# Kernel tuning notes

Hardware: AMD Instinct MI355X
Metric: run time of the kernel (lower is better)

The kernel has to match this reference:

```python
import jax, jax.numpy as jnp
import numpy as np

B, N, C = 4, 4096, 256
GROUPS = 50
M_SCALE = 10.0


def setup_inputs() -> dict:
    key = jax.random.key(0)
    ks = jax.random.split(key, 6)
    s = 0.02
    return {
        "inputs": jax.random.normal(ks[0], (B, N, 1, C), dtype=jnp.float32),
        "W_sem": jax.random.normal(ks[1], (C, 128), dtype=jnp.float32) * s,
        "b_sem": jnp.zeros((128,), jnp.float32),
        "W_seg": jax.random.normal(ks[2], (128, GROUPS), dtype=jnp.float32) * s,
        "b_seg": jnp.zeros((GROUPS,), jnp.float32),
        "W_sim": jax.random.normal(ks[3], (C, 128), dtype=jnp.float32) * s,
        "b_sim": jnp.zeros((128,), jnp.float32),
        "W_conf": jax.random.normal(ks[4], (C, 128), dtype=jnp.float32) * s,
        "b_conf": jnp.zeros((128,), jnp.float32),
        "W_cl": jax.random.normal(ks[5], (128, 1), dtype=jnp.float32) * s,
        "b_cl": jnp.zeros((1,), jnp.float32),
    }


def reference(inputs, W_sem, b_sem, W_seg, b_seg, W_sim, b_sim,
              W_conf, b_conf, W_cl, b_cl):
    # 1x1 Conv2D on [B, N, 1, C] == per-point dense layer on channels.
    x = inputs[:, :, 0, :]  # [B, N, C]

    # Semantic segmentation head
    Fsem = jnp.einsum('bnc,cd->bnd', x, W_sem) + b_sem          # [B, N, 128]
    ptssemseg_logits = jnp.einsum('bnd,dg->bng', Fsem, W_seg) + b_seg  # [B, N, G]
    ptssemseg = jax.nn.softmax(ptssemseg_logits, axis=-1)

    # Similarity head: pairwise squared distances of Fsim rows
    Fsim = jnp.einsum('bnc,cd->bnd', x, W_sim) + b_sim          # [B, N, 128]
    r = jnp.sum(Fsim * Fsim, axis=2)                             # [B, N]
    gram = jnp.einsum('bnd,bmd->bnm', Fsim, Fsim)                # [B, N, N]
    D = r[:, :, None] - 2.0 * gram + r[:, None, :]               # [B, N, N]
    simmat_logits = jnp.maximum(M_SCALE * D, 0.0)

    # Confidence head
    Fconf = jnp.einsum('bnc,cd->bnd', x, W_conf) + b_conf        # [B, N, 128]
    conf_logits = jnp.einsum('bnd,do->bno', Fconf, W_cl) + b_cl  # [B, N, 1]
    conf = jax.nn.sigmoid(conf_logits)

    return (ptssemseg, ptssemseg_logits, simmat_logits, conf, conf_logits)
```

## Files before the change

kernel.cpp:

```cpp
#include <hip/hip_runtime.h>
#include <cstdint>
#include <cstddef>

#define NN 4096
#define CC 256
#define GG 50

#define O_OUT1 819200
#define O_OUT2 1638400
#define O_OUT3 68747264
#define O_OUT4 68763648

typedef _Float16 half8 __attribute__((ext_vector_type(8)));
typedef float f32x4 __attribute__((ext_vector_type(4)));
typedef short short8 __attribute__((ext_vector_type(8)));

__device__ __forceinline__ unsigned bf16b(float f) {
    unsigned u = __float_as_uint(f);
    return (u + 0x7FFFu + ((u >> 16) & 1u)) >> 16;
}
__device__ __forceinline__ float bf16f(short s) {
    return __uint_as_float(((unsigned)(unsigned short)s) << 16);
}

__global__ __launch_bounds__(256) void k_proj(
    const float* __restrict__ x,
    const float* __restrict__ Wsem, const float* __restrict__ bsem,
    const float* __restrict__ Wseg, const float* __restrict__ bseg,
    const float* __restrict__ Wsim, const float* __restrict__ bsim,
    const float* __restrict__ Wconf, const float* __restrict__ bconf,
    const float* __restrict__ Wcl, const float* __restrict__ bcl,
    unsigned* __restrict__ fsimu, float* __restrict__ rnorm,
    float* __restrict__ out0, float* __restrict__ out1,
    float* __restrict__ out3, float* __restrict__ out4)
{
    __shared__ float hsem[64 * 132];
    __shared__ float confl[64], rns[64];

    int t = threadIdx.x;
    int lane = t & 63, wv = t >> 6;
    int rowl = lane & 15, quad = lane >> 4;
    int pbase = blockIdx.x * 64;

    if (t < 64) { confl[t] = 0.f; rns[t] = 0.f; }

    const float* wcol[6];
    #pragma unroll
    for (int jf = 0; jf < 6; ++jf) {
        int j384 = (wv * 6 + jf) * 16 + rowl;
        const float* m = (j384 < 128) ? Wsim : (j384 < 256) ? Wsem : Wconf;
        wcol[jf] = m + (j384 & 127);
    }
    const float* xrow[4];
    #pragma unroll
    for (int pf = 0; pf < 4; ++pf)
        xrow[pf] = x + (size_t)(pbase + pf * 16 + rowl) * CC;

    f32x4 acc[6][4];
    #pragma unroll
    for (int jf = 0; jf < 6; ++jf)
        #pragma unroll
        for (int pf = 0; pf < 4; ++pf) { f32x4 z = {0.f,0.f,0.f,0.f}; acc[jf][pf] = z; }

    #pragma unroll 2
    for (int kc = 0; kc < 8; ++kc) {
        half8 A[6];
        #pragma unroll
        for (int jf = 0; jf < 6; ++jf) {
            const float* wp = wcol[jf] + (size_t)(kc * 32 + quad * 8) * 128;
            #pragma unroll
            for (int e = 0; e < 8; ++e) A[jf][e] = (_Float16)wp[(size_t)e * 128];
        }
        half8 Bv[4];
        #pragma unroll
        for (int pf = 0; pf < 4; ++pf) {
            const float* xp = xrow[pf] + kc * 32 + quad * 8;
            float4 x0 = *(const float4*)xp;
            float4 x1 = *(const float4*)(xp + 4);
            Bv[pf][0] = (_Float16)x0.x; Bv[pf][1] = (_Float16)x0.y;
            Bv[pf][2] = (_Float16)x0.z; Bv[pf][3] = (_Float16)x0.w;
            Bv[pf][4] = (_Float16)x1.x; Bv[pf][5] = (_Float16)x1.y;
            Bv[pf][6] = (_Float16)x1.z; Bv[pf][7] = (_Float16)x1.w;
        }
        #pragma unroll
        for (int pf = 0; pf < 4; ++pf)
            #pragma unroll
            for (int jf = 0; jf < 6; ++jf)
                acc[jf][pf] = __builtin_amdgcn_mfma_f32_16x16x32_f16(A[jf], Bv[pf], acc[jf][pf], 0, 0, 0);
    }

    __syncthreads();

    float rsum[4] = {0.f,0.f,0.f,0.f};
    float csum[4] = {0.f,0.f,0.f,0.f};
    bool hasSim = (wv * 6 < 8);
    bool hasConf = (wv * 6 + 5 >= 16);

    #pragma unroll
    for (int jf = 0; jf < 6; ++jf) {
        int jfg = wv * 6 + jf;
        int j0 = jfg * 16 + quad * 4;
        const float* barr = (j0 < 128) ? (bsim + j0)
                          : (j0 < 256) ? (bsem + (j0 - 128)) : (bconf + (j0 - 256));
        float4 b4 = *(const float4*)barr;
        if (jfg < 8) {
            #pragma unroll
            for (int pf = 0; pf < 4; ++pf) {
                int pt = pf * 16 + rowl;
                f32x4 v = acc[jf][pf];
                unsigned p0 = bf16b(v[0] + b4.x) | (bf16b(v[1] + b4.y) << 16);
                unsigned p1 = bf16b(v[2] + b4.z) | (bf16b(v[3] + b4.w) << 16);
                *(uint2*)&fsimu[(size_t)(pbase + pt) * 64 + jfg * 8 + quad * 2] = make_uint2(p0, p1);
                float f0 = bf16f((short)(p0 & 0xFFFF)), f1 = bf16f((short)(p0 >> 16));
                float f2 = bf16f((short)(p1 & 0xFFFF)), f3 = bf16f((short)(p1 >> 16));
                rsum[pf] += f0*f0 + f1*f1 + f2*f2 + f3*f3;
            }
        } else if (jfg < 16) {
            #pragma unroll
            for (int pf = 0; pf < 4; ++pf) {
                int pt = pf * 16 + rowl;
                f32x4 v = acc[jf][pf];
                f32x4 o;
                o[0] = v[0] + b4.x; o[1] = v[1] + b4.y; o[2] = v[2] + b4.z; o[3] = v[3] + b4.w;
                *(f32x4*)&hsem[pt * 132 + (jfg - 8) * 16 + quad * 4] = o;
            }
        } else {
            float4 w4 = *(const float4*)&Wcl[(jfg - 16) * 16 + quad * 4];
            #pragma unroll
            for (int pf = 0; pf < 4; ++pf) {
                f32x4 v = acc[jf][pf];
                csum[pf] += (v[0] + b4.x) * w4.x + (v[1] + b4.y) * w4.y
                          + (v[2] + b4.z) * w4.z + (v[3] + b4.w) * w4.w;
            }
        }
    }
    if (hasSim) {
        #pragma unroll
        for (int pf = 0; pf < 4; ++pf) atomicAdd(&rns[pf * 16 + rowl], rsum[pf]);
    }
    if (hasConf) {
        #pragma unroll
        for (int pf = 0; pf < 4; ++pf) atomicAdd(&confl[pf * 16 + rowl], csum[pf]);
    }
    __syncthreads();

    if (t < 64) {
        float cl = confl[t] + bcl[0];
        out4[pbase + t] = cl;
        out3[pbase + t] = 1.f / (1.f + __expf(-cl));
        rnorm[pbase + t] = rns[t];
    }

    half8 As[4][4];
    #pragma unroll
    for (int gf = 0; gf < 4; ++gf) {
        int gg = gf * 16 + rowl;
        #pragma unroll
        for (int k2 = 0; k2 < 4; ++k2)
            #pragma unroll
            for (int e = 0; e < 8; ++e) {
                int d = k2 * 32 + quad * 8 + e;
                As[gf][k2][e] = (gg < GG) ? (_Float16)Wseg[(size_t)d * GG + gg] : (_Float16)0.f;
            }
    }
    f32x4 sacc[4];
    #pragma unroll
    for (int gf = 0; gf < 4; ++gf) { f32x4 z = {0.f,0.f,0.f,0.f}; sacc[gf] = z; }
    #pragma unroll
    for (int k2 = 0; k2 < 4; ++k2) {
        const float* hp = &hsem[(wv * 16 + rowl) * 132 + k2 * 32 + quad * 8];
        half8 Bh;
        #pragma unroll
        for (int e = 0; e < 8; ++e) Bh[e] = (_Float16)hp[e];
        #pragma unroll
        for (int gf = 0; gf < 4; ++gf)
            sacc[gf] = __builtin_amdgcn_mfma_f32_16x16x32_f16(As[gf][k2], Bh, sacc[gf], 0, 0, 0);
    }

    float l[4][4];
    float mx = -1e30f;
    #pragma unroll
    for (int gf = 0; gf < 4; ++gf)
        #pragma unroll
        for (int e = 0; e < 4; ++e) {
            int g = gf * 16 + quad * 4 + e;
            float lv = (g < GG) ? sacc[gf][e] + bseg[g] : -1e30f;
            l[gf][e] = lv;
            mx = fmaxf(mx, lv);
        }
    mx = fmaxf(mx, __shfl_xor(mx, 16));
    mx = fmaxf(mx, __shfl_xor(mx, 32));
    float s = 0.f;
    #pragma unroll
    for (int gf = 0; gf < 4; ++gf)
        #pragma unroll
        for (int e = 0; e < 4; ++e) {
            int g = gf * 16 + quad * 4 + e;
            if (g < GG) s += __expf(l[gf][e] - mx);
        }
    s += __shfl_xor(s, 16);
    s += __shfl_xor(s, 32);
    float inv = 1.f / s;

    size_t orow = (size_t)(pbase + wv * 16 + rowl) * GG;
    #pragma unroll
    for (int gf = 0; gf < 4; ++gf)
        #pragma unroll
        for (int e = 0; e < 4; ++e) {
            int g = gf * 16 + quad * 4 + e;
            if (g < GG) {
                out1[orow + g] = l[gf][e];
                out0[orow + g] = __expf(l[gf][e] - mx) * inv;
            }
        }
}

__global__ __launch_bounds__(256) void k_simmat(
    const short* __restrict__ fs, const float* __restrict__ rn, float* __restrict__ out2)
{
    int t = threadIdx.x;
    int lane = t & 63, wv = t >> 6;
    int b = blockIdx.y;

    int p = blockIdx.x;
    int tj = (int)((sqrtf((float)(8 * p + 1)) - 1.f) * 0.5f);
    while ((tj + 1) * (tj + 2) / 2 <= p) ++tj;
    while (tj * (tj + 1) / 2 > p) --tj;
    int ti = p - tj * (tj + 1) / 2;

    int I = ti * 128 + (wv >> 1) * 64;
    int J = tj * 128 + (wv & 1) * 64;
    int rowl = lane & 15, quad = lane >> 4;

    const short8* F = (const short8*)(fs + (size_t)b * NN * 128);
    const float* rb = rn + b * NN;

    f32x4 acc[4][4];
    #pragma unroll
    for (int r = 0; r < 4; ++r)
        #pragma unroll
        for (int c = 0; c < 4; ++c) { f32x4 z = {0.f,0.f,0.f,0.f}; acc[r][c] = z; }

    #pragma unroll
    for (int s = 0; s < 4; ++s) {
        short8 av[4], bv[4];
        #pragma unroll
        for (int r = 0; r < 4; ++r)
            av[r] = F[(size_t)(I + r * 16 + rowl) * 16 + s * 4 + quad];
        #pragma unroll
        for (int c = 0; c < 4; ++c)
            bv[c] = F[(size_t)(J + c * 16 + rowl) * 16 + s * 4 + quad];
        #pragma unroll
        for (int r = 0; r < 4; ++r)
            #pragma unroll
            for (int c = 0; c < 4; ++c)
                acc[r][c] = __builtin_amdgcn_mfma_f32_16x16x32_bf16(av[r], bv[c], acc[r][c], 0, 0, 0);
    }

    f32x4 rI4[4];
    float rJs[4];
    #pragma unroll
    for (int r = 0; r < 4; ++r)
        rI4[r] = *(const f32x4*)&rb[I + r * 16 + quad * 4];
    #pragma unroll
    for (int c = 0; c < 4; ++c)
        rJs[c] = rb[J + c * 16 + rowl];

    #pragma unroll
    for (int r = 0; r < 4; ++r)
        #pragma unroll
        for (int c = 0; c < 4; ++c) {
            f32x4 v = acc[r][c];
            float rj = rJs[c];
            f32x4 o;
            #pragma unroll
            for (int e = 0; e < 4; ++e)
                o[e] = fmaxf(10.f * (rI4[r][e] + rj) - 20.f * v[e], 0.f);
            acc[r][c] = o;
        }

    float* ob = out2 + (size_t)b * NN * NN;

    #pragma unroll
    for (int r = 0; r < 4; ++r) {
        int rbase = I + r * 16 + quad * 4;
        #pragma unroll
        for (int c = 0; c < 4; ++c) {
            int col = J + c * 16 + rowl;
            f32x4 v = acc[r][c];
            #pragma unroll
            for (int e = 0; e < 4; ++e)
                __builtin_nontemporal_store(v[e], &ob[(size_t)(rbase + e) * NN + col]);
        }
    }

    if (ti != tj) {
        #pragma unroll
        for (int c = 0; c < 4; ++c) {
            size_t rowoff = (size_t)(J + c * 16 + rowl) * NN;
            #pragma unroll
            for (int r = 0; r < 4; ++r)
                __builtin_nontemporal_store(acc[r][c],
                    (f32x4*)&ob[rowoff + (I + r * 16 + quad * 4)]);
        }
    }
}

extern "C" void kernel_launch(void* const* d_in, const int* in_sizes, int n_in,
                              void* d_out, int out_size, void* d_ws, size_t ws_size,
                              hipStream_t stream)
{
    const float* x     = (const float*)d_in[0];
    const float* Wsem  = (const float*)d_in[1];
    const float* bsem  = (const float*)d_in[2];
    const float* Wseg  = (const float*)d_in[3];
    const float* bseg  = (const float*)d_in[4];
    const float* Wsim  = (const float*)d_in[5];
    const float* bsim  = (const float*)d_in[6];
    const float* Wconf = (const float*)d_in[7];
    const float* bconf = (const float*)d_in[8];
    const float* Wcl   = (const float*)d_in[9];
    const float* bcl   = (const float*)d_in[10];

    const size_t FSIM_BYTES = (size_t)4 * NN * 128 * 2;
    if (ws_size < FSIM_BYTES + (size_t)4 * NN * sizeof(float)) return;
    unsigned* fsim = (unsigned*)d_ws;
    float* rnorm = (float*)((char*)d_ws + FSIM_BYTES);

    float* out  = (float*)d_out;
    float* out0 = out;
    float* out1 = out + O_OUT1;
    float* out2 = out + O_OUT2;
    float* out3 = out + O_OUT3;
    float* out4 = out + O_OUT4;

    hipLaunchKernelGGL(k_proj, dim3(256), dim3(256), 0, stream,
                       x, Wsem, bsem, Wseg, bseg, Wsim, bsim, Wconf, bconf, Wcl, bcl,
                       fsim, rnorm, out0, out1, out3, out4);
    hipLaunchKernelGGL(k_simmat, dim3(528, 4, 1), dim3(256), 0, stream,
                       (const short*)fsim, rnorm, out2);
}
```

Before: 357.9 us.

## Compute full row strips of simmat and stage through LDS for coalesced stores

Measured after the change: 415.5 us. 16.1% more time.

```diff
diff --git a/kernel.cpp b/kernel.cpp
--- a/kernel.cpp
+++ b/kernel.cpp
@@ -218,91 +218,67 @@
 __global__ __launch_bounds__(256) void k_simmat(
     const short* __restrict__ fs, const float* __restrict__ rn, float* __restrict__ out2)
 {
+    __shared__ float tile[16 * 516];
+
     int t = threadIdx.x;
     int lane = t & 63, wv = t >> 6;
+    int rowl = lane & 15, quad = lane >> 4;
     int b = blockIdx.y;
-
-    int p = blockIdx.x;
-    int tj = (int)((sqrtf((float)(8 * p + 1)) - 1.f) * 0.5f);
-    while ((tj + 1) * (tj + 2) / 2 <= p) ++tj;
-    while (tj * (tj + 1) / 2 > p) --tj;
-    int ti = p - tj * (tj + 1) / 2;
-
-    int I = ti * 128 + (wv >> 1) * 64;
-    int J = tj * 128 + (wv & 1) * 64;
-    int rowl = lane & 15, quad = lane >> 4;
+    int I = blockIdx.x * 16;
 
     const short8* F = (const short8*)(fs + (size_t)b * NN * 128);
     const float* rb = rn + b * NN;
-
-    f32x4 acc[4][4];
-    #pragma unroll
-    for (int r = 0; r < 4; ++r)
-        #pragma unroll
-        for (int c = 0; c < 4; ++c) { f32x4 z = {0.f,0.f,0.f,0.f}; acc[r][c] = z; }
-
-    #pragma unroll
-    for (int s = 0; s < 4; ++s) {
-        short8 av[4], bv[4];
-        #pragma unroll
-        for (int r = 0; r < 4; ++r)
-            av[r] = F[(size_t)(I + r * 16 + rowl) * 16 + s * 4 + quad];
-        #pragma unroll
-        for (int c = 0; c < 4; ++c)
-            bv[c] = F[(size_t)(J + c * 16 + rowl) * 16 + s * 4 + quad];
-        #pragma unroll
-        for (int r = 0; r < 4; ++r)
-            #pragma unroll
-            for (int c = 0; c < 4; ++c)
-                acc[r][c] = __builtin_amdgcn_mfma_f32_16x16x32_bf16(av[r], bv[c], acc[r][c], 0, 0, 0);
-    }
-
-    f32x4 rI4[4];
-    float rJs[4];
-    #pragma unroll
-    for (int r = 0; r < 4; ++r)
-        rI4[r] = *(const f32x4*)&rb[I + r * 16 + quad * 4];
-    #pragma unroll
-    for (int c = 0; c < 4; ++c)
-        rJs[c] = rb[J + c * 16 + rowl];
-
-    #pragma unroll
-    for (int r = 0; r < 4; ++r)
-        #pragma unroll
-        for (int c = 0; c < 4; ++c) {
-            f32x4 v = acc[r][c];
-            float rj = rJs[c];
-            f32x4 o;
-            #pragma unroll
-            for (int e = 0; e < 4; ++e)
-                o[e] = fmaxf(10.f * (rI4[r][e] + rj) - 20.f * v[e], 0.f);
-            acc[r][c] = o;
-        }
-
     float* ob = out2 + (size_t)b * NN * NN;
 
-    #pragma unroll
-    for (int r = 0; r < 4; ++r) {
-        int rbase = I + r * 16 + quad * 4;
-        #pragma unroll
-        for (int c = 0; c < 4; ++c) {
-            int col = J + c * 16 + rowl;
-            f32x4 v = acc[r][c];
-            #pragma unroll
-            for (int e = 0; e < 4; ++e)
-                __builtin_nontemporal_store(v[e], &ob[(size_t)(rbase + e) * NN + col]);
-        }
-    }
-
-    if (ti != tj) {
-        #pragma unroll
-        for (int c = 0; c < 4; ++c) {
-            size_t rowoff = (size_t)(J + c * 16 + rowl) * NN;
-            #pragma unroll
-            for (int r = 0; r < 4; ++r)
-                __builtin_nontemporal_store(acc[r][c],
-                    (f32x4*)&ob[rowoff + (I + r * 16 + quad * 4)]);
-        }
+    short8 av[4];
+    #pragma unroll
+    for (int s = 0; s < 4; ++s)
+        av[s] = F[(size_t)(I + rowl) * 16 + s * 4 + quad];
+
+    f32x4 rI = *(const f32x4*)&rb[I + quad * 4];
+
+    for (int cb = 0; cb < NN; cb += 512) {
+        int c0 = cb + wv * 128;
+
+        f32x4 acc[8];
+        #pragma unroll
+        for (int c = 0; c < 8; ++c) { f32x4 z = {0.f,0.f,0.f,0.f}; acc[c] = z; }
+
+        #pragma unroll
+        for (int s = 0; s < 4; ++s) {
+            short8 bv[8];
+            #pragma unroll
+            for (int c = 0; c < 8; ++c)
+                bv[c] = F[(size_t)(c0 + c * 16 + rowl) * 16 + s * 4 + quad];
+            #pragma unroll
+            for (int c = 0; c < 8; ++c)
+                acc[c] = __builtin_amdgcn_mfma_f32_16x16x32_bf16(av[s], bv[c], acc[c], 0, 0, 0);
+        }
+
+        #pragma unroll
+        for (int c = 0; c < 8; ++c) {
+            float rj = rb[c0 + c * 16 + rowl];
+            f32x4 v = acc[c];
+            int coff = wv * 128 + c * 16 + rowl;
+            #pragma unroll
+            for (int e = 0; e < 4; ++e) {
+                float dv = fmaxf(10.f * (rI[e] + rj) - 20.f * v[e], 0.f);
+                tile[(quad * 4 + e) * 516 + coff] = dv;
+            }
+        }
+        __syncthreads();
+
+        #pragma unroll
+        for (int rr = 0; rr < 4; ++rr) {
+            int row = wv * 4 + rr;
+            const f32x4* lp = (const f32x4*)&tile[row * 516];
+            f32x4 v0 = lp[lane];
+            f32x4 v1 = lp[64 + lane];
+            size_t go = (size_t)(I + row) * NN + cb;
+            __builtin_nontemporal_store(v0, (f32x4*)&ob[go + lane * 4]);
+            __builtin_nontemporal_store(v1, (f32x4*)&ob[go + 256 + lane * 4]);
+        }
+        __syncthreads();
     }
 }
 
@@ -337,6 +313,6 @@
     hipLaunchKernelGGL(k_proj, dim3(256), dim3(256), 0, stream,
                        x, Wsem, bsem, Wseg, bseg, Wsim, bsim, Wconf, bconf, Wcl, bcl,
                        fsim, rnorm, out0, out1, out3, out4);
-    hipLaunchKernelGGL(k_simmat, dim3(528, 4, 1), dim3(256), 0, stream,
+    hipLaunchKernelGGL(k_simmat, dim3(256, 4), dim3(256), 0, stream,
                        (const short*)fsim, rnorm, out2);
 }
```
